# Optimization experiments

Measured on AMD Instinct MI355X. Metric: run time of the kernel, lower is better.

Reference implementation:

```python
import jax, jax.numpy as jnp
import numpy as np

B, S, D, H = 2, 2048, 1024, 16
DK = D // H


def setup_inputs() -> dict:
    key = jax.random.key(0)
    ks = jax.random.split(key, 12)
    s = 1.0 / np.sqrt(D)
    return {
        "query": jax.random.normal(ks[0], (B, S, D), dtype=jnp.float32),
        "key": jax.random.normal(ks[1], (B, S, D), dtype=jnp.float32),
        "value": jax.random.normal(ks[2], (B, S, D), dtype=jnp.float32),
        "mask": jax.random.randint(ks[3], (B, 1, 1, S), 0, 2, dtype=jnp.int32),
        "wq": jax.random.normal(ks[4], (D, D), dtype=jnp.float32) * s,
        "bq": jnp.zeros((D,), dtype=jnp.float32),
        "wk": jax.random.normal(ks[5], (D, D), dtype=jnp.float32) * s,
        "bk": jnp.zeros((D,), dtype=jnp.float32),
        "wv": jax.random.normal(ks[6], (D, D), dtype=jnp.float32) * s,
        "bv": jnp.zeros((D,), dtype=jnp.float32),
        "wo": jax.random.normal(ks[7], (D, D), dtype=jnp.float32) * s,
        "bo": jnp.zeros((D,), dtype=jnp.float32),
    }


def reference(query, key, value, mask, wq, bq, wk, bk, wv, bv, wo, bo):
    b, s, d = query.shape
    # torch Linear: y = x @ W^T + b, then split heads -> [B, H, S, dk]
    def proj(x, w, bias):
        return (x @ w.T + bias).reshape(b, -1, H, DK).transpose(0, 2, 1, 3)

    q = proj(query, wq, bq)
    k = proj(key, wk, bk)
    v = proj(value, wv, bv)

    scores = jnp.einsum("bhqd,bhkd->bhqk", q, k) / jnp.sqrt(jnp.float32(DK))
    scores = jnp.where(mask == 0, jnp.float32(-1e9), scores)
    attn = jax.nn.softmax(scores, axis=-1)  # [B,H,S,S]
    x = jnp.einsum("bhqk,bhkd->bhqd", attn, v)
    x = x.transpose(0, 2, 1, 3).reshape(b, s, d)
    return x @ wo.T + bo
```

## Files before the change

### kernel.cpp

```cpp
#include <hip/hip_runtime.h>
#include <math.h>

#define B_  2
#define S_  2048
#define D_  1024
#define H_  16
#define DK_ 64

typedef unsigned short u16;
typedef unsigned int u32;
typedef __bf16 bf16x8 __attribute__((ext_vector_type(8)));
typedef float f32x4 __attribute__((ext_vector_type(4)));
typedef float f32x16 __attribute__((ext_vector_type(16)));
typedef u32 u32x2 __attribute__((ext_vector_type(2)));
typedef u32 u32x4 __attribute__((ext_vector_type(4)));

typedef const __attribute__((address_space(1))) void* gas1_t;
typedef __attribute__((address_space(3))) void* las3_t;

__device__ __forceinline__ void gload_lds16(const void* g, void* l) {
    __builtin_amdgcn_global_load_lds((gas1_t)g, (las3_t)l, 16, 0, 0);
}

__device__ __forceinline__ u16 f2bf(float f) {
    union { float f; unsigned u; } v; v.f = f;
    return (u16)((v.u + 0x7fffu + ((v.u >> 16) & 1u)) >> 16);
}

__device__ __forceinline__ u32 pack_bf16_2(float lo, float hi) {
    union { float f; u32 u; } a, b;
    a.f = lo; b.f = hi;
    return __builtin_amdgcn_perm(b.u + 0x8000u, a.u + 0x8000u, 0x07060302u);
}

__device__ __forceinline__ u32 cvtpk_bf16(float lo, float hi) {
    u32 r;
    asm("v_cvt_pk_bf16_f32 %0, %1, %2" : "=v"(r) : "v"(lo), "v"(hi));
    return r;
}

__global__ __launch_bounds__(256)
void cast_all(const float* __restrict__ q, const float* __restrict__ k,
              const float* __restrict__ v, const float* __restrict__ wq,
              const float* __restrict__ wk, const float* __restrict__ wv,
              const float* __restrict__ wo, const int* __restrict__ mask,
              u16* __restrict__ qb, u16* __restrict__ kb, u16* __restrict__ vb,
              u16* __restrict__ wqb, u16* __restrict__ wkb, u16* __restrict__ wvb,
              u16* __restrict__ wob, float* __restrict__ mfac,
              float* __restrict__ nmaskf)
{
    const int bi = blockIdx.x;
    const int tid = threadIdx.x;
    if (bi >= 2064) {
        const int b = bi - 2064;
        __shared__ int red[256];
        int c = 0;
#pragma unroll
        for (int j = 0; j < 8; ++j)
            c += (mask[b * S_ + tid * 8 + j] == 0) ? 1 : 0;
        red[tid] = c;
        __syncthreads();
        for (int s = 128; s > 0; s >>= 1) {
            if (tid < s) red[tid] += red[tid + s];
            __syncthreads();
        }
        if (tid == 0) nmaskf[b] = (float)red[0];
        return;
    }
    if (bi >= 2048) {
        const int idx = (bi - 2048) * 256 + tid;
        mfac[idx] = mask[idx] ? 1.0f : 0.0f;
        return;
    }
#pragma unroll
    for (int j = 0; j < 8; ++j) {
        const int i = bi * 256 + tid + j * 524288;
        const float* src; u16* dst; int off;
        if (i < 3 * 1048576) {
            const int seg = i >> 20; off = i & 1048575;
            src = (seg == 0) ? q : (seg == 1) ? k : v;
            dst = (seg == 0) ? qb : (seg == 1) ? kb : vb;
        } else {
            const int jj = i - 3 * 1048576;
            const int seg = jj >> 18; off = jj & 262143;
            src = (seg == 0) ? wq : (seg == 1) ? wk : (seg == 2) ? wv : wo;
            dst = (seg == 0) ? wqb : (seg == 1) ? wkb : (seg == 2) ? wvb : wob;
        }
        const float4 val = ((const float4*)src)[off];
        uint2 o;
        o.x = pack_bf16_2(val.x, val.y);
        o.y = pack_bf16_2(val.z, val.w);
        ((uint2*)dst)[off] = o;
    }
}

template<int BN>
__device__ __forceinline__ void gemm_body(
    const u16* __restrict__ A, const u16* __restrict__ W,
    const float* __restrict__ bias, void* __restrict__ outp,
    float scale, int mode, int m0, int n0,
    const float* __restrict__ rowfac, const float* __restrict__ colfac)
{
    constexpr int NJ = BN / 32;
    __shared__ u16 sA[128 * 64];
    __shared__ u16 sW[BN * 64];

    const int tid  = threadIdx.x;
    const int wave = tid >> 6, lane = tid & 63;
    const int quad = lane >> 4, l16 = lane & 15;
    const int wm = (wave >> 1) * 64;
    const int wn = (wave & 1) * (BN / 2);
    const int srow = lane >> 3;
    const int scol = ((lane & 7) ^ srow) * 8;
    const int sw7  = l16 & 7;

    f32x4 acc[4][NJ];
    const f32x4 zero = {0.f, 0.f, 0.f, 0.f};
#pragma unroll
    for (int i = 0; i < 4; ++i)
#pragma unroll
        for (int j = 0; j < NJ; ++j) acc[i][j] = zero;

    const u16* ast = A + (size_t)(m0 + wave * 8 + srow) * D_ + scol;
    const u16* wst = W + (size_t)(n0 + wave * 8 + srow) * D_ + scol;

    for (int k0 = 0; k0 < D_; k0 += 64) {
#pragma unroll
        for (int t = 0; t < 4; ++t)
            gload_lds16(ast + (size_t)t * 32 * D_ + k0, sA + (wave + t * 4) * 512);
        if (BN == 128) {
#pragma unroll
            for (int t = 0; t < 4; ++t)
                gload_lds16(wst + (size_t)t * 32 * D_ + k0, sW + (wave + t * 4) * 512);
        } else {
#pragma unroll
            for (int t = 0; t < 2; ++t)
                gload_lds16(wst + (size_t)t * 32 * D_ + k0, sW + (wave + t * 4) * 512);
        }
        __syncthreads();

#pragma unroll
        for (int kh = 0; kh < 2; ++kh) {
            const int phys = ((kh * 4 + quad) ^ sw7) * 8;
            bf16x8 af[4], bfr[NJ];
#pragma unroll
            for (int i = 0; i < 4; ++i)
                af[i] = *(const bf16x8*)(sA + (wm + i * 16 + l16) * 64 + phys);
#pragma unroll
            for (int j = 0; j < NJ; ++j)
                bfr[j] = *(const bf16x8*)(sW + (wn + j * 16 + l16) * 64 + phys);
#pragma unroll
            for (int i = 0; i < 4; ++i)
#pragma unroll
                for (int j = 0; j < NJ; ++j)
                    acc[i][j] = __builtin_amdgcn_mfma_f32_16x16x32_bf16(af[i], bfr[j], acc[i][j], 0, 0, 0);
        }
        __syncthreads();
    }

#pragma unroll
    for (int i = 0; i < 4; ++i) {
        float rf4[4];
        if (mode == 1 && rowfac) {
#pragma unroll
            for (int r = 0; r < 4; ++r)
                rf4[r] = rowfac[m0 + wm + i * 16 + quad * 4 + r];
        }
#pragma unroll
        for (int j = 0; j < NJ; ++j) {
            const int n = n0 + wn + j * 16 + l16;
            if (mode == 3) {
                const float cf = colfac ? colfac[n] : 1.0f;
#pragma unroll
                for (int r = 0; r < 4; ++r) {
                    const int mp = m0 + wm + i * 16 + quad * 4 + r;
                    ((u16*)outp)[(size_t)mp * (B_ * S_) + n] = f2bf((acc[i][j][r] + bias[mp]) * cf);
                }
            } else {
                const float bn = bias[n];
#pragma unroll
                for (int r = 0; r < 4; ++r) {
                    const int m = m0 + wm + i * 16 + quad * 4 + r;
                    float v = acc[i][j][r] + bn;
                    if (mode == 0) {
                        ((float*)outp)[(size_t)m * D_ + n] = v;
                    } else {
                        v *= scale;
                        if (rowfac) v *= rf4[r];
                        const int b = m >> 11, s = m & (S_ - 1);
                        const int h = n >> 6, dk = n & 63;
                        ((u16*)outp)[(((size_t)(b * H_ + h)) * S_ + s) * DK_ + dk] = f2bf(v);
                    }
                }
            }
        }
    }
}

__global__ __launch_bounds__(256)
void qkv_gemm(const u16* __restrict__ qin, const u16* __restrict__ kin, const u16* __restrict__ vin,
              const u16* __restrict__ wqb, const u16* __restrict__ wkb, const u16* __restrict__ wvb,
              const float* __restrict__ bq, const float* __restrict__ bk, const float* __restrict__ bv,
              u16* __restrict__ Qp, u16* __restrict__ Kp, u16* __restrict__ Vt,
              const float* __restrict__ mfac)
{
    const int z = blockIdx.z;
    if (z == 2) {
        gemm_body<128>(wvb, vin, bv, Vt, 1.0f, 3, blockIdx.x * 128, blockIdx.y * 128,
                       nullptr, mfac);
    } else {
        const u16* A = (z == 0) ? qin : kin;
        const u16* W = (z == 0) ? wqb : wkb;
        const float* bias = (z == 0) ? bq : bk;
        u16* outp = (z == 0) ? Qp : Kp;
        const float scale = (z == 0) ? 0.18033688011112042f : 1.0f;
        const float* rf = (z == 1) ? mfac : nullptr;
        gemm_body<128>(A, W, bias, outp, scale, 1, blockIdx.y * 128, blockIdx.x * 128,
                       rf, nullptr);
    }
}

__global__ __launch_bounds__(256)
void out_gemm(const u16* __restrict__ Xc, const u16* __restrict__ wob,
              const float* __restrict__ bo, float* __restrict__ out)
{
    gemm_body<64>(Xc, wob, bo, out, 1.0f, 0, blockIdx.y * 128, blockIdx.x * 64,
                  nullptr, nullptr);
}

__global__ __launch_bounds__(512, 4)
void attn_mfma(const u16* __restrict__ Qp, const u16* __restrict__ Kp,
               const u16* __restrict__ Vt, const float* __restrict__ nmaskf,
               u16* __restrict__ Xc)
{
    __shared__ u16 sKV[2][2][8192];

    const int tid  = threadIdx.x;
    const int wave = tid >> 6, lane = tid & 63;
    const int qg = wave & 3, kg = wave >> 2;
    const int l31 = lane & 31, hi = lane >> 5;
    const int qt = blockIdx.x & 15;
    const int bh = blockIdx.x >> 4;
    const int b  = bh >> 4;
    const int h  = bh & 15;
    const int lr  = lane >> 3;
    const int cl  = (lane & 7) ^ lr;
    const int sw5 = l31 & 7;

    const u16* Qb = Qp + ((size_t)bh * S_ + qt * 128) * DK_;
    const u16* Kb = Kp + (size_t)bh * S_ * DK_;
    const int vdk = (qg * 8 + lr) + 32 * (cl >> 2);
    const u16* Vsrc = Vt + (size_t)(h * 64 + vdk) * (B_ * S_) + b * S_ + (cl & 3) * 8;
    const u16* Ksrc = Kb + (size_t)(qg * 8 + lr) * DK_ + cl * 8;

    bf16x8 qf[4];
    {
        const u16* qrow = Qb + (size_t)(qg * 32 + l31) * DK_ + hi * 8;
        qf[0] = *(const bf16x8*)(qrow);
        qf[1] = *(const bf16x8*)(qrow + 16);
        qf[2] = *(const bf16x8*)(qrow + 32);
        qf[3] = *(const bf16x8*)(qrow + 48);
    }

    const u16* kpre = Ksrc + (size_t)kg * 64 * DK_;
    const u16* vpre = Vsrc + kg * 64;
    {
        u16* dst = sKV[kg][0];
        gload_lds16(kpre,                    dst + qg * 512);
        gload_lds16(kpre + (size_t)32 * DK_, dst + 2048 + qg * 512);
        gload_lds16(vpre,                    dst + 4096 + qg * 512);
        gload_lds16(vpre + 32,               dst + 6144 + qg * 512);
        kpre += (size_t)128 * DK_;
        vpre += 128;
    }

    f32x16 oc[2];
    const f32x16 z16 = {0.f,0.f,0.f,0.f,0.f,0.f,0.f,0.f,
                        0.f,0.f,0.f,0.f,0.f,0.f,0.f,0.f};
    oc[0] = z16; oc[1] = z16;
    float lsum = 0.f;

    for (int i = 0; i < 16; ++i) {
        __syncthreads();
        const int cur = i & 1;

        if (i < 15) {
            u16* dst = sKV[kg][cur ^ 1];
            gload_lds16(kpre,                    dst + qg * 512);
            gload_lds16(kpre + (size_t)32 * DK_, dst + 2048 + qg * 512);
            gload_lds16(vpre,                    dst + 4096 + qg * 512);
            gload_lds16(vpre + 32,               dst + 6144 + qg * 512);
            kpre += (size_t)128 * DK_;
            vpre += 128;
        }
        const u16* sKA = sKV[kg][cur];
        const u16* sKB = sKA + 2048;
        const u16* sVA = sKA + 4096;
        const u16* sVB = sKA + 6144;

        f32x16 sfrA, sfrB;
        {
            const bf16x8 a0 = *(const bf16x8*)(sKA + l31 * 64 + (((0 + hi) ^ sw5)) * 8);
            const bf16x8 a1 = *(const bf16x8*)(sKA + l31 * 64 + (((2 + hi) ^ sw5)) * 8);
            const bf16x8 a2 = *(const bf16x8*)(sKA + l31 * 64 + (((4 + hi) ^ sw5)) * 8);
            const bf16x8 a3 = *(const bf16x8*)(sKA + l31 * 64 + (((6 + hi) ^ sw5)) * 8);
            const bf16x8 b0 = *(const bf16x8*)(sKB + l31 * 64 + (((0 + hi) ^ sw5)) * 8);
            const bf16x8 b1 = *(const bf16x8*)(sKB + l31 * 64 + (((2 + hi) ^ sw5)) * 8);
            const bf16x8 b2 = *(const bf16x8*)(sKB + l31 * 64 + (((4 + hi) ^ sw5)) * 8);
            const bf16x8 b3 = *(const bf16x8*)(sKB + l31 * 64 + (((6 + hi) ^ sw5)) * 8);
            __builtin_amdgcn_s_setprio(1);
            sfrA = __builtin_amdgcn_mfma_f32_32x32x16_bf16(a0, qf[0], z16, 0, 0, 0);
            sfrB = __builtin_amdgcn_mfma_f32_32x32x16_bf16(b0, qf[0], z16, 0, 0, 0);
            sfrA = __builtin_amdgcn_mfma_f32_32x32x16_bf16(a1, qf[1], sfrA, 0, 0, 0);
            sfrB = __builtin_amdgcn_mfma_f32_32x32x16_bf16(b1, qf[1], sfrB, 0, 0, 0);
            sfrA = __builtin_amdgcn_mfma_f32_32x32x16_bf16(a2, qf[2], sfrA, 0, 0, 0);
            sfrB = __builtin_amdgcn_mfma_f32_32x32x16_bf16(b2, qf[2], sfrB, 0, 0, 0);
            sfrA = __builtin_amdgcn_mfma_f32_32x32x16_bf16(a3, qf[3], sfrA, 0, 0, 0);
            sfrB = __builtin_amdgcn_mfma_f32_32x32x16_bf16(b3, qf[3], sfrB, 0, 0, 0);
            __builtin_amdgcn_s_setprio(0);
        }

        {
            float p[16];
#pragma unroll
            for (int r = 0; r < 16; ++r) p[r] = __builtin_amdgcn_exp2f(sfrA[r]);
            const float s0 = (p[0] + p[1]) + (p[2] + p[3]);
            const float s1 = (p[4] + p[5]) + (p[6] + p[7]);
            const float s2 = (p[8] + p[9]) + (p[10] + p[11]);
            const float s3 = (p[12] + p[13]) + (p[14] + p[15]);
            lsum += (s0 + s1) + (s2 + s3);
            const u32 W00 = cvtpk_bf16(p[0], p[1]);
            const u32 W01 = cvtpk_bf16(p[2], p[3]);
            const u32 W10 = cvtpk_bf16(p[4], p[5]);
            const u32 W11 = cvtpk_bf16(p[6], p[7]);
            const u32 W20 = cvtpk_bf16(p[8], p[9]);
            const u32 W21 = cvtpk_bf16(p[10], p[11]);
            const u32 W30 = cvtpk_bf16(p[12], p[13]);
            const u32 W31 = cvtpk_bf16(p[14], p[15]);
            const u32x2 e0 = __builtin_amdgcn_permlane32_swap(W00, W10, false, false);
            const u32x2 e1 = __builtin_amdgcn_permlane32_swap(W01, W11, false, false);
            const u32x2 e2 = __builtin_amdgcn_permlane32_swap(W20, W30, false, false);
            const u32x2 e3 = __builtin_amdgcn_permlane32_swap(W21, W31, false, false);
            u32x4 A0 = { e0[0], e1[0], e0[1], e1[1] };
            u32x4 A1 = { e2[0], e3[0], e2[1], e3[1] };
            const bf16x8 pa0 = *(const bf16x8*)&A0;
            const bf16x8 pa1 = *(const bf16x8*)&A1;
            const bf16x8 v00 = *(const bf16x8*)(sVA + l31 * 64 + (((0 + hi) ^ sw5)) * 8);
            const bf16x8 v01 = *(const bf16x8*)(sVA + l31 * 64 + (((2 + hi) ^ sw5)) * 8);
            const bf16x8 v10 = *(const bf16x8*)(sVA + l31 * 64 + (((4 + hi) ^ sw5)) * 8);
            const bf16x8 v11 = *(const bf16x8*)(sVA + l31 * 64 + (((6 + hi) ^ sw5)) * 8);
            __builtin_amdgcn_s_setprio(1);
            oc[0] = __builtin_amdgcn_mfma_f32_32x32x16_bf16(pa0, v00, oc[0], 0, 0, 0);
            oc[1] = __builtin_amdgcn_mfma_f32_32x32x16_bf16(pa0, v10, oc[1], 0, 0, 0);
            oc[0] = __builtin_amdgcn_mfma_f32_32x32x16_bf16(pa1, v01, oc[0], 0, 0, 0);
            oc[1] = __builtin_amdgcn_mfma_f32_32x32x16_bf16(pa1, v11, oc[1], 0, 0, 0);
            __builtin_amdgcn_s_setprio(0);
        }

        {
            float p[16];
#pragma unroll
            for (int r = 0; r < 16; ++r) p[r] = __builtin_amdgcn_exp2f(sfrB[r]);
            const float s0 = (p[0] + p[1]) + (p[2] + p[3]);
            const float s1 = (p[4] + p[5]) + (p[6] + p[7]);
            const float s2 = (p[8] + p[9]) + (p[10] + p[11]);
            const float s3 = (p[12] + p[13]) + (p[14] + p[15]);
            lsum += (s0 + s1) + (s2 + s3);
            const u32 W00 = cvtpk_bf16(p[0], p[1]);
            const u32 W01 = cvtpk_bf16(p[2], p[3]);
            const u32 W10 = cvtpk_bf16(p[4], p[5]);
            const u32 W11 = cvtpk_bf16(p[6], p[7]);
            const u32 W20 = cvtpk_bf16(p[8], p[9]);
            const u32 W21 = cvtpk_bf16(p[10], p[11]);
            const u32 W30 = cvtpk_bf16(p[12], p[13]);
            const u32 W31 = cvtpk_bf16(p[14], p[15]);
            const u32x2 e0 = __builtin_amdgcn_permlane32_swap(W00, W10, false, false);
            const u32x2 e1 = __builtin_amdgcn_permlane32_swap(W01, W11, false, false);
            const u32x2 e2 = __builtin_amdgcn_permlane32_swap(W20, W30, false, false);
            const u32x2 e3 = __builtin_amdgcn_permlane32_swap(W21, W31, false, false);
            u32x4 A0 = { e0[0], e1[0], e0[1], e1[1] };
            u32x4 A1 = { e2[0], e3[0], e2[1], e3[1] };
            const bf16x8 pa0 = *(const bf16x8*)&A0;
            const bf16x8 pa1 = *(const bf16x8*)&A1;
            const bf16x8 v00 = *(const bf16x8*)(sVB + l31 * 64 + (((0 + hi) ^ sw5)) * 8);
            const bf16x8 v01 = *(const bf16x8*)(sVB + l31 * 64 + (((2 + hi) ^ sw5)) * 8);
            const bf16x8 v10 = *(const bf16x8*)(sVB + l31 * 64 + (((4 + hi) ^ sw5)) * 8);
            const bf16x8 v11 = *(const bf16x8*)(sVB + l31 * 64 + (((6 + hi) ^ sw5)) * 8);
            __builtin_amdgcn_s_setprio(1);
            oc[0] = __builtin_amdgcn_mfma_f32_32x32x16_bf16(pa0, v00, oc[0], 0, 0, 0);
            oc[1] = __builtin_amdgcn_mfma_f32_32x32x16_bf16(pa0, v10, oc[1], 0, 0, 0);
            oc[0] = __builtin_amdgcn_mfma_f32_32x32x16_bf16(pa1, v01, oc[0], 0, 0, 0);
            oc[1] = __builtin_amdgcn_mfma_f32_32x32x16_bf16(pa1, v11, oc[1], 0, 0, 0);
            __builtin_amdgcn_s_setprio(0);
        }
    }

    {
        union { float f; u32 u; } lu; lu.f = lsum;
        const u32x2 lr2 = __builtin_amdgcn_permlane32_swap(lu.u, lu.u, false, false);
        union { u32 u; float f; } pu; pu.u = hi ? lr2[0] : lr2[1];
        lsum += pu.f;
    }

    __syncthreads();
    float* sO = (float*)&sKV[0][0][0];
    float* sL = (float*)((char*)sO + 32768);
    if (hi == 0) sL[kg * 128 + qg * 32 + l31] = lsum;
    if (kg == 1) {
#pragma unroll
        for (int dh = 0; dh < 2; ++dh)
#pragma unroll
            for (int g = 0; g < 4; ++g) {
                f32x4 t = { oc[dh][g * 4 + 0], oc[dh][g * 4 + 1],
                            oc[dh][g * 4 + 2], oc[dh][g * 4 + 3] };
                *(f32x4*)(sO + qg * 2048 + ((dh * 4 + g) * 2 + hi) * 128 + l31 * 4) = t;
            }
    }
    __syncthreads();
    if (kg == 0) {
        const float nm = nmaskf[b];
#pragma unroll
        for (int g = 0; g < 4; ++g) {
            const f32x4 oA = *(const f32x4*)(sO + qg * 2048 + ((0 + g) * 2 + hi) * 128 + l31 * 4);
            const f32x4 oB = *(const f32x4*)(sO + qg * 2048 + ((4 + g) * 2 + hi) * 128 + l31 * 4);
#pragma unroll
            for (int rr = 0; rr < 4; ++rr) {
                const int qrow = rr + 8 * g + 4 * hi;
                const float inv = __builtin_amdgcn_rcpf(
                    sL[qg * 32 + qrow] + sL[128 + qg * 32 + qrow] - nm);
                const int s = qt * 128 + qg * 32 + qrow;
                const size_t base = ((size_t)(b * S_ + s)) * D_ + h * 64 + l31;
                Xc[base]      = f2bf((oc[0][g * 4 + rr] + oA[rr]) * inv);
                Xc[base + 32] = f2bf((oc[1][g * 4 + rr] + oB[rr]) * inv);
            }
        }
    }
}

extern "C" void kernel_launch(void* const* d_in, const int* in_sizes, int n_in,
                              void* d_out, int out_size, void* d_ws, size_t ws_size,
                              hipStream_t stream)
{
    (void)in_sizes; (void)n_in; (void)out_size; (void)ws_size;

    const float* query = (const float*)d_in[0];
    const float* key   = (const float*)d_in[1];
    const float* value = (const float*)d_in[2];
    const int*   mask  = (const int*)d_in[3];
    const float* wq    = (const float*)d_in[4];
    const float* bq    = (const float*)d_in[5];
    const float* wk    = (const float*)d_in[6];
    const float* bk    = (const float*)d_in[7];
    const float* wv    = (const float*)d_in[8];
    const float* bv    = (const float*)d_in[9];
    const float* wo    = (const float*)d_in[10];
    const float* bo    = (const float*)d_in[11];

    const size_t NE = (size_t)B_ * S_ * D_;
    const size_t WE = (size_t)D_ * D_;

    u16* qb  = (u16*)d_ws;
    u16* kb  = qb + NE;
    u16* vb  = kb + NE;
    u16* wqb = vb + NE;
    u16* wkb = wqb + WE;
    u16* wvb = wkb + WE;
    u16* wob = wvb + WE;
    u16* Qp  = wob + WE;
    u16* Kp  = Qp + NE;
    u16* Vt  = Kp + NE;
    float* mfac   = (float*)(Vt + NE);
    float* nmaskf = mfac + 4096;
    u16* Xc  = qb;

    cast_all<<<2066, 256, 0, stream>>>(query, key, value, wq, wk, wv, wo, mask,
                                       qb, kb, vb, wqb, wkb, wvb, wob, mfac, nmaskf);

    qkv_gemm<<<dim3(D_ / 128, (B_ * S_) / 128, 3), 256, 0, stream>>>(
        qb, kb, vb, wqb, wkb, wvb, bq, bk, bv, Qp, Kp, Vt, mfac);

    attn_mfma<<<dim3(B_ * H_ * (S_ / 128)), 512, 0, stream>>>(Qp, Kp, Vt, nmaskf, Xc);

    out_gemm<<<dim3(D_ / 64, (B_ * S_) / 128), 256, 0, stream>>>(Xc, wob, bo, (float*)d_out);
}
```

Measured before the change: 221.0 us.

## Double-buffer GEMM LDS tiles and swizzle block IDs across XCDs

The GEMM main loop now uses two LDS buffers, so the global-to-LDS load of the next K tile is issued before the MFMA work on the current tile, and there is one barrier per iteration instead of two. Separately, all three kernels now launch a flat 1D grid and remap block IDs so that consecutive tiles land on the same XCD (stride-8 swizzle), aiming for better L2 locality. Double buffering doubles GEMM shared memory use, which may lower occupancy.

```diff
diff --git a/kernel.cpp b/kernel.cpp
--- a/kernel.cpp
+++ b/kernel.cpp
@@ -102,8 +102,8 @@
     const float* __restrict__ rowfac, const float* __restrict__ colfac)
 {
     constexpr int NJ = BN / 32;
-    __shared__ u16 sA[128 * 64];
-    __shared__ u16 sW[BN * 64];
+    __shared__ u16 sA[2][128 * 64];
+    __shared__ u16 sW[2][BN * 64];
 
     const int tid  = threadIdx.x;
     const int wave = tid >> 6, lane = tid & 63;
@@ -124,20 +124,26 @@
     const u16* ast = A + (size_t)(m0 + wave * 8 + srow) * D_ + scol;
     const u16* wst = W + (size_t)(n0 + wave * 8 + srow) * D_ + scol;
 
-    for (int k0 = 0; k0 < D_; k0 += 64) {
-#pragma unroll
-        for (int t = 0; t < 4; ++t)
-            gload_lds16(ast + (size_t)t * 32 * D_ + k0, sA + (wave + t * 4) * 512);
-        if (BN == 128) {
+#pragma unroll
+    for (int t = 0; t < 4; ++t)
+        gload_lds16(ast + (size_t)t * 32 * D_, sA[0] + (wave + t * 4) * 512);
+#pragma unroll
+    for (int t = 0; t < BN / 32; ++t)
+        gload_lds16(wst + (size_t)t * 32 * D_, sW[0] + (wave + t * 4) * 512);
+
+    for (int it = 0; it < 16; ++it) {
+        __syncthreads();
+        const int cur = it & 1;
+
+        if (it < 15) {
+            const int k0 = (it + 1) * 64;
 #pragma unroll
             for (int t = 0; t < 4; ++t)
-                gload_lds16(wst + (size_t)t * 32 * D_ + k0, sW + (wave + t * 4) * 512);
-        } else {
-#pragma unroll
-            for (int t = 0; t < 2; ++t)
-                gload_lds16(wst + (size_t)t * 32 * D_ + k0, sW + (wave + t * 4) * 512);
-        }
-        __syncthreads();
+                gload_lds16(ast + (size_t)t * 32 * D_ + k0, sA[cur ^ 1] + (wave + t * 4) * 512);
+#pragma unroll
+            for (int t = 0; t < BN / 32; ++t)
+                gload_lds16(wst + (size_t)t * 32 * D_ + k0, sW[cur ^ 1] + (wave + t * 4) * 512);
+        }
 
 #pragma unroll
         for (int kh = 0; kh < 2; ++kh) {
@@ -145,17 +151,16 @@
             bf16x8 af[4], bfr[NJ];
 #pragma unroll
             for (int i = 0; i < 4; ++i)
-                af[i] = *(const bf16x8*)(sA + (wm + i * 16 + l16) * 64 + phys);
+                af[i] = *(const bf16x8*)(sA[cur] + (wm + i * 16 + l16) * 64 + phys);
 #pragma unroll
             for (int j = 0; j < NJ; ++j)
-                bfr[j] = *(const bf16x8*)(sW + (wn + j * 16 + l16) * 64 + phys);
+                bfr[j] = *(const bf16x8*)(sW[cur] + (wn + j * 16 + l16) * 64 + phys);
 #pragma unroll
             for (int i = 0; i < 4; ++i)
 #pragma unroll
                 for (int j = 0; j < NJ; ++j)
                     acc[i][j] = __builtin_amdgcn_mfma_f32_16x16x32_bf16(af[i], bfr[j], acc[i][j], 0, 0, 0);
         }
-        __syncthreads();
     }
 
 #pragma unroll
@@ -204,9 +209,15 @@
               u16* __restrict__ Qp, u16* __restrict__ Kp, u16* __restrict__ Vt,
               const float* __restrict__ mfac)
 {
-    const int z = blockIdx.z;
+    const int bid = blockIdx.x;
+    const int swz = (bid & 7) * 96 + (bid >> 3);
+    const int z   = swz >> 8;
+    const int rem = swz & 255;
+    const int by  = rem >> 3;
+    const int bx  = rem & 7;
+
     if (z == 2) {
-        gemm_body<128>(wvb, vin, bv, Vt, 1.0f, 3, blockIdx.x * 128, blockIdx.y * 128,
+        gemm_body<128>(wvb, vin, bv, Vt, 1.0f, 3, bx * 128, by * 128,
                        nullptr, mfac);
     } else {
         const u16* A = (z == 0) ? qin : kin;
@@ -215,7 +226,7 @@
         u16* outp = (z == 0) ? Qp : Kp;
         const float scale = (z == 0) ? 0.18033688011112042f : 1.0f;
         const float* rf = (z == 1) ? mfac : nullptr;
-        gemm_body<128>(A, W, bias, outp, scale, 1, blockIdx.y * 128, blockIdx.x * 128,
+        gemm_body<128>(A, W, bias, outp, scale, 1, by * 128, bx * 128,
                        rf, nullptr);
     }
 }
@@ -224,7 +235,11 @@
 void out_gemm(const u16* __restrict__ Xc, const u16* __restrict__ wob,
               const float* __restrict__ bo, float* __restrict__ out)
 {
-    gemm_body<64>(Xc, wob, bo, out, 1.0f, 0, blockIdx.y * 128, blockIdx.x * 64,
+    const int bid = blockIdx.x;
+    const int swz = (bid & 7) * 64 + (bid >> 3);
+    const int by  = swz >> 4;
+    const int bx  = swz & 15;
+    gemm_body<64>(Xc, wob, bo, out, 1.0f, 0, by * 128, bx * 64,
                   nullptr, nullptr);
 }
 
@@ -239,8 +254,10 @@
     const int wave = tid >> 6, lane = tid & 63;
     const int qg = wave & 3, kg = wave >> 2;
     const int l31 = lane & 31, hi = lane >> 5;
-    const int qt = blockIdx.x & 15;
-    const int bh = blockIdx.x >> 4;
+    const int bid = blockIdx.x;
+    const int swz = (bid & 7) * 64 + (bid >> 3);
+    const int qt = swz & 15;
+    const int bh = swz >> 4;
     const int b  = bh >> 4;
     const int h  = bh & 15;
     const int lr  = lane >> 3;
@@ -476,10 +493,10 @@
     cast_all<<<2066, 256, 0, stream>>>(query, key, value, wq, wk, wv, wo, mask,
                                        qb, kb, vb, wqb, wkb, wvb, wob, mfac, nmaskf);
 
-    qkv_gemm<<<dim3(D_ / 128, (B_ * S_) / 128, 3), 256, 0, stream>>>(
+    qkv_gemm<<<768, 256, 0, stream>>>(
         qb, kb, vb, wqb, wkb, wvb, bq, bk, bv, Qp, Kp, Vt, mfac);
 
-    attn_mfma<<<dim3(B_ * H_ * (S_ / 128)), 512, 0, stream>>>(Qp, Kp, Vt, nmaskf, Xc);
-
-    out_gemm<<<dim3(D_ / 64, (B_ * S_) / 128), 256, 0, stream>>>(Xc, wob, bo, (float*)d_out);
-}
+    attn_mfma<<<512, 512, 0, stream>>>(Qp, Kp, Vt, nmaskf, Xc);
+
+    out_gemm<<<512, 256, 0, stream>>>(Xc, wob, bo, (float*)d_out);
+}
```

Measured after the change: 224.0 us. No clear change (+1.4%).

## Shrink GEMM M-tiles to 64 and add XCD-aware block swizzling to all kernels

Applied to the files above, without the earlier changes.

Makes the GEMM body generic over BM, and uses 64-row tiles in the QKV and output projections, which doubles the block count so more of the 256 CUs are filled. It also launches each kernel as a 1D grid with a stride-8 block remap, so consecutive logical tiles land on the same XCD and can share its L2. The cost is less operand reuse per tile, since each W tile is loaded by twice as many blocks.

```diff
diff --git a/kernel.cpp b/kernel.cpp
--- a/kernel.cpp
+++ b/kernel.cpp
@@ -94,30 +94,31 @@
     }
 }
 
-template<int BN>
+template<int BM, int BN>
 __device__ __forceinline__ void gemm_body(
     const u16* __restrict__ A, const u16* __restrict__ W,
     const float* __restrict__ bias, void* __restrict__ outp,
     float scale, int mode, int m0, int n0,
     const float* __restrict__ rowfac, const float* __restrict__ colfac)
 {
+    constexpr int MI = BM / 32;
     constexpr int NJ = BN / 32;
-    __shared__ u16 sA[128 * 64];
+    __shared__ u16 sA[BM * 64];
     __shared__ u16 sW[BN * 64];
 
     const int tid  = threadIdx.x;
     const int wave = tid >> 6, lane = tid & 63;
     const int quad = lane >> 4, l16 = lane & 15;
-    const int wm = (wave >> 1) * 64;
+    const int wm = (wave >> 1) * (BM / 2);
     const int wn = (wave & 1) * (BN / 2);
     const int srow = lane >> 3;
     const int scol = ((lane & 7) ^ srow) * 8;
     const int sw7  = l16 & 7;
 
-    f32x4 acc[4][NJ];
+    f32x4 acc[MI][NJ];
     const f32x4 zero = {0.f, 0.f, 0.f, 0.f};
 #pragma unroll
-    for (int i = 0; i < 4; ++i)
+    for (int i = 0; i < MI; ++i)
 #pragma unroll
         for (int j = 0; j < NJ; ++j) acc[i][j] = zero;
 
@@ -126,31 +127,25 @@
 
     for (int k0 = 0; k0 < D_; k0 += 64) {
 #pragma unroll
-        for (int t = 0; t < 4; ++t)
+        for (int t = 0; t < BM / 32; ++t)
             gload_lds16(ast + (size_t)t * 32 * D_ + k0, sA + (wave + t * 4) * 512);
-        if (BN == 128) {
-#pragma unroll
-            for (int t = 0; t < 4; ++t)
-                gload_lds16(wst + (size_t)t * 32 * D_ + k0, sW + (wave + t * 4) * 512);
-        } else {
-#pragma unroll
-            for (int t = 0; t < 2; ++t)
-                gload_lds16(wst + (size_t)t * 32 * D_ + k0, sW + (wave + t * 4) * 512);
-        }
+#pragma unroll
+        for (int t = 0; t < BN / 32; ++t)
+            gload_lds16(wst + (size_t)t * 32 * D_ + k0, sW + (wave + t * 4) * 512);
         __syncthreads();
 
 #pragma unroll
         for (int kh = 0; kh < 2; ++kh) {
             const int phys = ((kh * 4 + quad) ^ sw7) * 8;
-            bf16x8 af[4], bfr[NJ];
-#pragma unroll
-            for (int i = 0; i < 4; ++i)
+            bf16x8 af[MI], bfr[NJ];
+#pragma unroll
+            for (int i = 0; i < MI; ++i)
                 af[i] = *(const bf16x8*)(sA + (wm + i * 16 + l16) * 64 + phys);
 #pragma unroll
             for (int j = 0; j < NJ; ++j)
                 bfr[j] = *(const bf16x8*)(sW + (wn + j * 16 + l16) * 64 + phys);
 #pragma unroll
-            for (int i = 0; i < 4; ++i)
+            for (int i = 0; i < MI; ++i)
 #pragma unroll
                 for (int j = 0; j < NJ; ++j)
                     acc[i][j] = __builtin_amdgcn_mfma_f32_16x16x32_bf16(af[i], bfr[j], acc[i][j], 0, 0, 0);
@@ -159,7 +154,7 @@
     }
 
 #pragma unroll
-    for (int i = 0; i < 4; ++i) {
+    for (int i = 0; i < MI; ++i) {
         float rf4[4];
         if (mode == 1 && rowfac) {
 #pragma unroll
@@ -204,19 +199,26 @@
               u16* __restrict__ Qp, u16* __restrict__ Kp, u16* __restrict__ Vt,
               const float* __restrict__ mfac)
 {
-    const int z = blockIdx.z;
+    const int bid = blockIdx.x;
+    const int swz = (bid & 7) * 192 + (bid >> 3);
+    const int z   = swz >> 9;
+    const int rem = swz & 511;
+
     if (z == 2) {
-        gemm_body<128>(wvb, vin, bv, Vt, 1.0f, 3, blockIdx.x * 128, blockIdx.y * 128,
-                       nullptr, mfac);
+        const int mi = rem & 15, ni = rem >> 4;
+        gemm_body<64, 128>(wvb, vin, bv, Vt, 1.0f, 3, mi * 64, ni * 128,
+                           nullptr, mfac);
     } else {
+        const int by = rem >> 3;
+        const int bx = rem & 7;
         const u16* A = (z == 0) ? qin : kin;
         const u16* W = (z == 0) ? wqb : wkb;
         const float* bias = (z == 0) ? bq : bk;
         u16* outp = (z == 0) ? Qp : Kp;
         const float scale = (z == 0) ? 0.18033688011112042f : 1.0f;
         const float* rf = (z == 1) ? mfac : nullptr;
-        gemm_body<128>(A, W, bias, outp, scale, 1, blockIdx.y * 128, blockIdx.x * 128,
-                       rf, nullptr);
+        gemm_body<64, 128>(A, W, bias, outp, scale, 1, by * 64, bx * 128,
+                           rf, nullptr);
     }
 }
 
@@ -224,8 +226,12 @@
 void out_gemm(const u16* __restrict__ Xc, const u16* __restrict__ wob,
               const float* __restrict__ bo, float* __restrict__ out)
 {
-    gemm_body<64>(Xc, wob, bo, out, 1.0f, 0, blockIdx.y * 128, blockIdx.x * 64,
-                  nullptr, nullptr);
+    const int bid = blockIdx.x;
+    const int swz = (bid & 7) * 128 + (bid >> 3);
+    const int by  = swz >> 4;
+    const int bx  = swz & 15;
+    gemm_body<64, 64>(Xc, wob, bo, out, 1.0f, 0, by * 64, bx * 64,
+                      nullptr, nullptr);
 }
 
 __global__ __launch_bounds__(512, 4)
@@ -239,8 +245,10 @@
     const int wave = tid >> 6, lane = tid & 63;
     const int qg = wave & 3, kg = wave >> 2;
     const int l31 = lane & 31, hi = lane >> 5;
-    const int qt = blockIdx.x & 15;
-    const int bh = blockIdx.x >> 4;
+    const int bid = blockIdx.x;
+    const int swz = (bid & 7) * 64 + (bid >> 3);
+    const int qt = swz & 15;
+    const int bh = swz >> 4;
     const int b  = bh >> 4;
     const int h  = bh & 15;
     const int lr  = lane >> 3;
@@ -476,10 +484,10 @@
     cast_all<<<2066, 256, 0, stream>>>(query, key, value, wq, wk, wv, wo, mask,
                                        qb, kb, vb, wqb, wkb, wvb, wob, mfac, nmaskf);
 
-    qkv_gemm<<<dim3(D_ / 128, (B_ * S_) / 128, 3), 256, 0, stream>>>(
+    qkv_gemm<<<1536, 256, 0, stream>>>(
         qb, kb, vb, wqb, wkb, wvb, bq, bk, bv, Qp, Kp, Vt, mfac);
 
-    attn_mfma<<<dim3(B_ * H_ * (S_ / 128)), 512, 0, stream>>>(Qp, Kp, Vt, nmaskf, Xc);
-
-    out_gemm<<<dim3(D_ / 64, (B_ * S_) / 128), 256, 0, stream>>>(Xc, wob, bo, (float*)d_out);
-}
+    attn_mfma<<<512, 512, 0, stream>>>(Qp, Kp, Vt, nmaskf, Xc);
+
+    out_gemm<<<1024, 256, 0, stream>>>(Xc, wob, bo, (float*)d_out);
+}
```

After: 211.1 us. 1.05x faster.
